# Kernel optimization log

Hardware: AMD Instinct MI355X
Metric: run time of the kernel (lower is better)

Reference implementation:

```python
import jax, jax.numpy as jnp
import numpy as np

NUM_HEADS = 16
ROPE_BASE = 10000.0


def _rope_cos_sin(T, head_dim, dtype):
    # standard rotary: angles[t, i] = t * base^(-2i/head_dim), half-split layout
    inv_freq = 1.0 / (ROPE_BASE ** (jnp.arange(0, head_dim, 2, dtype=jnp.float32) / head_dim))
    ang = jnp.arange(T, dtype=jnp.float32)[:, None] * inv_freq[None, :]  # [T, hd/2]
    cos = jnp.concatenate([jnp.cos(ang), jnp.cos(ang)], axis=-1).astype(dtype)  # [T, hd]
    sin = jnp.concatenate([jnp.sin(ang), jnp.sin(ang)], axis=-1).astype(dtype)
    return cos, sin


def _rotate_half(t):
    t1, t2 = jnp.split(t, 2, axis=-1)
    return jnp.concatenate([-t2, t1], axis=-1)


def _apply_rope(t, cos, sin):
    # t: [B, H, T, hd]; cos/sin: [T, hd]
    return t * cos[None, None] + _rotate_half(t) * sin[None, None]


def setup_inputs() -> dict:
    key = jax.random.key(0)
    B, T, C = 2, 2048, 1024
    k1, k2, k3 = jax.random.split(key, 3)
    x = jax.random.normal(k1, (B, T, C), dtype=jnp.float32)
    w_attn = jax.random.normal(k2, (C, 3 * C), dtype=jnp.float32) * (C ** -0.5)
    w_proj = jax.random.normal(k3, (C, C), dtype=jnp.float32) * (C ** -0.5)
    return {"x": x, "w_attn": w_attn, "w_proj": w_proj}


def reference(x, w_attn, w_proj):
    B, T, C = x.shape
    H = NUM_HEADS
    hd = C // H

    qkv = x @ w_attn  # [B, T, 3C]
    q, k, v = jnp.split(qkv, 3, axis=-1)
    # [B, T, C] -> [B, H, T, hd]
    q = q.reshape(B, T, H, hd).transpose(0, 2, 1, 3)
    k = k.reshape(B, T, H, hd).transpose(0, 2, 1, 3)
    v = v.reshape(B, T, H, hd).transpose(0, 2, 1, 3)

    cos, sin = _rope_cos_sin(T, hd, x.dtype)
    q = _apply_rope(q, cos, sin)
    k = _apply_rope(k, cos, sin)

    scale = 1.0 / np.sqrt(hd).astype(np.float32)
    att = jnp.einsum('bhqd,bhkd->bhqk', q, k) * scale  # [B, H, T, T]
    causal = jnp.tril(jnp.ones((T, T), dtype=bool))
    att = jnp.where(causal[None, None], att, jnp.array(-jnp.inf, dtype=att.dtype))
    att = jax.nn.softmax(att, axis=-1)
    y = jnp.einsum('bhqk,bhkd->bhqd', att, v)  # [B, H, T, hd]
    y = y.transpose(0, 2, 1, 3).reshape(B, T, C)
    return y @ w_proj
```

## Files before the change

### kernel.cpp

```cpp
#include <hip/hip_runtime.h>

typedef unsigned short u16;
typedef unsigned int u32;
typedef unsigned long long u64;
typedef __attribute__((ext_vector_type(8))) short s16x8;
typedef __attribute__((ext_vector_type(8))) __bf16 bf16x8;
typedef __attribute__((ext_vector_type(4))) float fx4;
typedef __attribute__((ext_vector_type(16))) float fx16;
typedef __attribute__((ext_vector_type(2))) u32 u32x2;
typedef __attribute__((ext_vector_type(4))) u32 u32x4;

__device__ __forceinline__ fx4 mfma_16x16x32(s16x8 a, s16x8 b, fx4 c) {
  return __builtin_amdgcn_mfma_f32_16x16x32_bf16(
      __builtin_bit_cast(bf16x8, a), __builtin_bit_cast(bf16x8, b), c, 0, 0, 0);
}
__device__ __forceinline__ fx16 mfma_32x32x16(s16x8 a, s16x8 b, fx16 c) {
  return __builtin_amdgcn_mfma_f32_32x32x16_bf16(
      __builtin_bit_cast(bf16x8, a), __builtin_bit_cast(bf16x8, b), c, 0, 0, 0);
}

__device__ __forceinline__ u16 f2bf(float f) {
  u32 u = __builtin_bit_cast(u32, f);
  u32 r = u + 0x7fffu + ((u >> 16) & 1u);
  return (u16)(r >> 16);
}
__device__ __forceinline__ float bf2f(u16 h) {
  u32 u = ((u32)h) << 16;
  return __builtin_bit_cast(float, u);
}

__device__ __forceinline__ u32 cvtpk(float lo, float hi) {
  u32 r;
  asm("v_cvt_pk_bf16_f32 %0, %1, %2" : "=v"(r) : "v"(lo), "v"(hi));
  return r;
}

__device__ __forceinline__ float max3f(float a, float b, float c) {
  float r;
  asm("v_max3_f32 %0, %1, %2, %3" : "=v"(r) : "v"(a), "v"(b), "v"(c));
  return r;
}

__device__ __forceinline__ void plswap(u32& x, u32& y) {
  typedef __attribute__((ext_vector_type(2))) unsigned int uix2;
  uix2 r = __builtin_amdgcn_permlane32_swap(x, y, false, false);
  x = r[0];
  y = r[1];
}

__device__ __forceinline__ float xhalf_max(float v) {
  u32 a = __builtin_bit_cast(u32, v), b = a;
  plswap(a, b);
  return fmaxf(__builtin_bit_cast(float, a), __builtin_bit_cast(float, b));
}
__device__ __forceinline__ float xhalf_sum(float v) {
  u32 a = __builtin_bit_cast(u32, v), b = a;
  plswap(a, b);
  return __builtin_bit_cast(float, a) + __builtin_bit_cast(float, b);
}

__device__ __forceinline__ void gload16(const void* g, void* l) {
  __builtin_amdgcn_global_load_lds(
      (const __attribute__((address_space(1))) u32*)g,
      (__attribute__((address_space(3))) u32*)l, 16, 0, 0);
}

#define B_ 2
#define T_ 2048
#define C_ 1024
#define H_ 16
#define HD_ 64
#define BH_ 32
#define M_ 4096
#define CF_ 0.18033688011112042f

__global__ __launch_bounds__(256) void prep_k(
    const float* __restrict__ x, const float* __restrict__ wa,
    const float* __restrict__ wp, u16* __restrict__ xb, u16* __restrict__ waT,
    u16* __restrict__ wpT, float* __restrict__ ct, float* __restrict__ st) {
  __shared__ u16 T_s[64 * 72];
  int b = blockIdx.x, tid = threadIdx.x;
  if (b < 2048) {
    int id = b * 256 + tid;
    const fx4* p = (const fx4*)(x + (u64)id * 8);
    fx4 v0 = p[0], v1 = p[1];
    s16x8 r;
#pragma unroll
    for (int j = 0; j < 4; ++j) {
      r[j] = (short)f2bf(v0[j]);
      r[4 + j] = (short)f2bf(v1[j]);
    }
    *((s16x8*)xb + id) = r;
  } else if (b < 3072) {
    const float* W;
    u16* WT;
    int Ncols, bx, by;
    if (b < 2816) {
      int i = b - 2048;
      W = wa; WT = waT; Ncols = 3072; bx = i % 48; by = i / 48;
    } else {
      int i = b - 2816;
      W = wp; WT = wpT; Ncols = 1024; bx = i % 16; by = i / 16;
    }
    int c0 = bx * 64, r0 = by * 64;
#pragma unroll
    for (int it = 0; it < 4; ++it) {
      int idx = it * 256 + tid;
      int r = idx >> 4, c4 = (idx & 15) * 4;
      fx4 v = *(const fx4*)(W + (u64)(r0 + r) * Ncols + c0 + c4);
#pragma unroll
      for (int j = 0; j < 4; ++j) T_s[(c4 + j) * 72 + r] = f2bf(v[j]);
    }
    __syncthreads();
#pragma unroll
    for (int it = 0; it < 2; ++it) {
      int idx = it * 256 + tid;
      int rc = idx >> 3, c8 = (idx & 7) * 8;
      s16x8 v = *(const s16x8*)(T_s + rc * 72 + c8);
      *(s16x8*)(WT + (u64)(c0 + rc) * 1024 + r0 + c8) = v;
    }
  } else {
    int id = (b - 3072) * 256 + tid;
    int t = id >> 5, i = id & 31;
    float f = exp2f(-(float)i * (13.287712379549449f / 32.0f));
    float a = (float)t * f;
    float s, c;
    sincosf(a, &s, &c);
    ct[id] = c;
    st[id] = s;
  }
}

__global__ __launch_bounds__(512, 2) void gemm1_8ph(
    const u16* __restrict__ A, const u16* __restrict__ B,
    u16* __restrict__ Qo, u16* __restrict__ Ko, u16* __restrict__ Vo,
    const float* __restrict__ ct, const float* __restrict__ st) {
  __shared__ u16 As[2][2][128 * 64];
  __shared__ u16 Bs[2][2][128 * 64];
  const int K = 1024;
  int tid = threadIdx.x, lane = tid & 63, w = tid >> 6;
  int wm = w >> 2, wn = w & 3, l15 = lane & 15, l4 = lane >> 4;
  int id = blockIdx.y * 12 + blockIdx.x;
  id = (id & 7) * 24 + (id >> 3);
  int m0 = (id / 12) * 256, n0 = (id % 12) * 256;

  const u16* asrc[2][2];
  const u16* bsrc[2][2];
  int dst16[2];
#pragma unroll
  for (int c = 0; c < 2; ++c) {
    int p = c * 512 + tid;
    int row = p >> 3, s = (p & 7) ^ (row & 7);
    dst16[c] = p * 16;
#pragma unroll
    for (int hh = 0; hh < 2; ++hh) {
      asrc[hh][c] = A + (u64)(m0 + hh * 128 + row) * K + s * 8;
      bsrc[hh][c] = B + (u64)(n0 + hh * 128 + row) * K + s * 8;
    }
  }

#define STAGE_A1(BUF, KOFF)                                               \
  do {                                                                    \
    _Pragma("unroll")                                                     \
    for (int hh_ = 0; hh_ < 2; ++hh_)                                     \
      _Pragma("unroll")                                                   \
      for (int c_ = 0; c_ < 2; ++c_)                                      \
        gload16(asrc[hh_][c_] + (KOFF), (char*)As[BUF][hh_] + dst16[c_]); \
  } while (0)
#define STAGE_B1(BUF, KOFF)                                               \
  do {                                                                    \
    _Pragma("unroll")                                                     \
    for (int hh_ = 0; hh_ < 2; ++hh_)                                     \
      _Pragma("unroll")                                                   \
      for (int c_ = 0; c_ < 2; ++c_)                                      \
        gload16(bsrc[hh_][c_] + (KOFF), (char*)Bs[BUF][hh_] + dst16[c_]); \
  } while (0)

#define RD_A(BUF, MI, KS)                                                  \
  (*(const s16x8*)((const char*)As[BUF][wm] +                              \
                   ((((MI)*16 + l15) * 8 +                                 \
                     (((KS)*4 + l4) ^ (l15 & 7))) * 16)))
#define RD_B(BUF, NJ, KS)                                                  \
  (*(const s16x8*)((const char*)Bs[BUF][wn >> 1] +                         \
                   ((((wn & 1) * 64 + (NJ)*16 + l15) * 8 +                 \
                     (((KS)*4 + l4) ^ (l15 & 7))) * 16)))

  fx4 acc[8][4] = {};

  STAGE_A1(0, 0);
  STAGE_B1(0, 0);
  asm volatile("s_waitcnt vmcnt(0)" ::: "memory");
  __builtin_amdgcn_s_barrier();
  __builtin_amdgcn_sched_barrier(0);

  for (int kt = 0; kt < 16; ++kt) {
    int buf = kt & 1;
    int ko = (kt + 1) * 64;
    s16x8 a[4], bb[4];
#pragma unroll
    for (int i = 0; i < 4; ++i) a[i] = RD_A(buf, i, 0);
#pragma unroll
    for (int j = 0; j < 4; ++j) bb[j] = RD_B(buf, j, 0);
    if (kt + 1 < 16) STAGE_A1(buf ^ 1, ko);
    __builtin_amdgcn_s_setprio(1);
#pragma unroll
    for (int i = 0; i < 4; ++i)
#pragma unroll
      for (int j = 0; j < 4; ++j)
        acc[i][j] = mfma_16x16x32(a[i], bb[j], acc[i][j]);
    __builtin_amdgcn_s_setprio(0);
    __builtin_amdgcn_s_barrier();
#pragma unroll
    for (int i = 0; i < 4; ++i) a[i] = RD_A(buf, 4 + i, 0);
    if (kt + 1 < 16) STAGE_B1(buf ^ 1, ko);
    __builtin_amdgcn_s_setprio(1);
#pragma unroll
    for (int i = 0; i < 4; ++i)
#pragma unroll
      for (int j = 0; j < 4; ++j)
        acc[4 + i][j] = mfma_16x16x32(a[i], bb[j], acc[4 + i][j]);
    __builtin_amdgcn_s_setprio(0);
    __builtin_amdgcn_s_barrier();
#pragma unroll
    for (int i = 0; i < 4; ++i) a[i] = RD_A(buf, i, 1);
#pragma unroll
    for (int j = 0; j < 4; ++j) bb[j] = RD_B(buf, j, 1);
    __builtin_amdgcn_s_setprio(1);
#pragma unroll
    for (int i = 0; i < 4; ++i)
#pragma unroll
      for (int j = 0; j < 4; ++j)
        acc[i][j] = mfma_16x16x32(a[i], bb[j], acc[i][j]);
    __builtin_amdgcn_s_setprio(0);
    __builtin_amdgcn_s_barrier();
#pragma unroll
    for (int i = 0; i < 4; ++i) a[i] = RD_A(buf, 4 + i, 1);
    __builtin_amdgcn_s_setprio(1);
#pragma unroll
    for (int i = 0; i < 4; ++i)
#pragma unroll
      for (int j = 0; j < 4; ++j)
        acc[4 + i][j] = mfma_16x16x32(a[i], bb[j], acc[4 + i][j]);
    __builtin_amdgcn_s_setprio(0);
    asm volatile("s_waitcnt vmcnt(0)" ::: "memory");
    __builtin_amdgcn_s_barrier();
    __builtin_amdgcn_sched_barrier(0);
  }
#undef STAGE_A1
#undef STAGE_B1
#undef RD_A
#undef RD_B

#pragma unroll
  for (int mi = 0; mi < 8; ++mi)
#pragma unroll
    for (int r = 0; r < 4; ++r) {
      int row = m0 + wm * 128 + mi * 16 + l4 * 4 + r;
      int b2 = row >> 11, t = row & (T_ - 1);
#pragma unroll
      for (int nj = 0; nj < 2; ++nj) {
        int col = n0 + wn * 64 + nj * 16 + l15;
        int qi = col >> 10, h = (col >> 6) & 15, d = nj * 16 + l15;
        float lo = acc[mi][nj][r], hi = acc[mi][nj + 2][r];
        if (qi == 2) {
          u64 vbase =
              ((((u64)(b2 * H_ + h)) * (T_ / 8) + (t >> 3)) * HD_ + d) * 8 + (t & 7);
          Vo[vbase] = f2bf(lo);
          Vo[vbase + 32 * 8] = f2bf(hi);
        } else {
          float c = ct[t * 32 + d], s = st[t * 32 + d];
          float sc = (qi == 0) ? CF_ : 1.0f;
          u16* dst = (qi == 0) ? Qo : Ko;
          u64 base = ((((u64)(b2 * H_ + h)) * 8 + (d >> 3)) * T_ + t) * 8 + (d & 7);
          dst[base] = f2bf((lo * c - hi * s) * sc);
          dst[base + (u64)4 * T_ * 8] = f2bf((hi * c + lo * s) * sc);
        }
      }
    }
}

__global__ __launch_bounds__(256, 3) void gemm2_k(
    const u16* __restrict__ A, const u16* __restrict__ B, float* __restrict__ C,
    int M, int N, int K) {
  __shared__ u16 AsS[3][128 * 32];
  __shared__ u16 BsS[3][128 * 32];
  int tid = threadIdx.x, lane = tid & 63, w = tid >> 6;
  int wm = w >> 1, wn = w & 1, l15 = lane & 15, l4 = lane >> 4;
  int nwg = gridDim.x * gridDim.y;
  int id = blockIdx.y * gridDim.x + blockIdx.x;
  int qq = nwg >> 3;
  id = (id & 7) * qq + (id >> 3);
  int m0 = (id / gridDim.x) * 128, n0 = (id % gridDim.x) * 128;
  fx4 acc[4][4] = {};

  const u16* asrc[2];
  const u16* bsrc[2];
#pragma unroll
  for (int g = 0; g < 2; ++g) {
    int idx = g * 256 + tid;
    int row = idx >> 2, slot = (idx & 3) ^ (row & 3);
    asrc[g] = A + (u64)(m0 + row) * K + slot * 8;
    bsrc[g] = B + (u64)(n0 + row) * K + slot * 8;
  }

#define GSTAGE(S, KOFF)                                                      \
  do {                                                                       \
    _Pragma("unroll")                                                        \
    for (int g_ = 0; g_ < 2; ++g_) {                                         \
      gload16(asrc[g_] + (KOFF), (char*)AsS[S] + g_ * 4096 + tid * 16);      \
      gload16(bsrc[g_] + (KOFF), (char*)BsS[S] + g_ * 4096 + tid * 16);      \
    }                                                                        \
  } while (0)

#define GCOMP(S)                                                             \
  do {                                                                       \
    s16x8 a_[4], b_[4];                                                      \
    _Pragma("unroll")                                                        \
    for (int mi_ = 0; mi_ < 4; ++mi_) {                                      \
      int r_ = wm * 64 + mi_ * 16 + l15;                                     \
      a_[mi_] = *(const s16x8*)((const char*)AsS[S] + r_ * 64 +              \
                                ((l4 ^ (r_ & 3)) * 16));                     \
    }                                                                        \
    _Pragma("unroll")                                                        \
    for (int ni_ = 0; ni_ < 4; ++ni_) {                                      \
      int r_ = wn * 64 + ni_ * 16 + l15;                                     \
      b_[ni_] = *(const s16x8*)((const char*)BsS[S] + r_ * 64 +              \
                                ((l4 ^ (r_ & 3)) * 16));                     \
    }                                                                        \
    _Pragma("unroll")                                                        \
    for (int mi_ = 0; mi_ < 4; ++mi_)                                        \
      _Pragma("unroll")                                                      \
      for (int ni_ = 0; ni_ < 4; ++ni_)                                      \
        acc[mi_][ni_] = mfma_16x16x32(a_[mi_], b_[ni_], acc[mi_][ni_]);      \
  } while (0)

  int NT = K >> 5;
  GSTAGE(0, 0);
  GSTAGE(1, 32);
  int s0 = 0, s1 = 1, s2 = 2;
  for (int t = 0; t < NT; ++t) {
    __builtin_amdgcn_s_barrier();
    __builtin_amdgcn_sched_barrier(0);
    if (t + 2 < NT) GSTAGE(s2, (t + 2) * 32);
    __builtin_amdgcn_sched_barrier(0);
    if (t < NT - 2)
      asm volatile("s_waitcnt vmcnt(8)" ::: "memory");
    else if (t == NT - 2)
      asm volatile("s_waitcnt vmcnt(4)" ::: "memory");
    else
      asm volatile("s_waitcnt vmcnt(0)" ::: "memory");
    __builtin_amdgcn_s_barrier();
    __builtin_amdgcn_sched_barrier(0);
    GCOMP(s0);
    int tmp = s0;
    s0 = s1;
    s1 = s2;
    s2 = tmp;
  }
#undef GSTAGE
#undef GCOMP

#pragma unroll
  for (int mi = 0; mi < 4; ++mi)
#pragma unroll
    for (int ni = 0; ni < 4; ++ni)
#pragma unroll
      for (int r = 0; r < 4; ++r) {
        u64 row = (u64)(m0 + wm * 64 + mi * 16 + l4 * 4 + r);
        int col = n0 + wn * 64 + ni * 16 + l15;
        C[row * N + col] = acc[mi][ni][r];
      }
}

#define LOADK(KC, KVI)                                                 \
  do {                                                                 \
    _Pragma("unroll")                                                  \
    for (int ks_ = 0; ks_ < 4; ++ks_)                                  \
      KC[ks_] = *(const s16x8*)(kp[ks_] + (u64)(KVI) * 256);           \
  } while (0)

#define LOADV(VC, KVI)                                                 \
  do {                                                                 \
    const u16* vk_ = vpb + (u64)(KVI) * 2048;                          \
    VC[0] = *(const s16x8*)(vk_);                                      \
    VC[1] = *(const s16x8*)(vk_ + 256);                                \
    VC[2] = *(const s16x8*)(vk_ + 1024);                               \
    VC[3] = *(const s16x8*)(vk_ + 1280);                               \
  } while (0)

#define ATTN_STEP(KC, VC, KVI)                                                \
  do {                                                                        \
    fx16 s_ = {};                                                             \
    __builtin_amdgcn_s_setprio(1);                                            \
    _Pragma("unroll")                                                         \
    for (int ks_ = 0; ks_ < 4; ++ks_)                                         \
      s_ = mfma_32x32x16(KC[ks_], qf[ks_], s_);                               \
    __builtin_amdgcn_s_setprio(0);                                            \
    if ((KVI) == jt) {                                                        \
      _Pragma("unroll")                                                       \
      for (int r_ = 0; r_ < 16; ++r_) {                                       \
        int cr_ = (r_ & 3) + 8 * (r_ >> 2) + 4 * h;                           \
        s_[r_] = (cr_ > ql) ? -1e30f : s_[r_];                                \
      }                                                                       \
    }                                                                         \
    float u0_ = max3f(s_[0], s_[1], s_[2]);                                   \
    float u1_ = max3f(s_[3], s_[4], s_[5]);                                   \
    float u2_ = max3f(s_[6], s_[7], s_[8]);                                   \
    float u3_ = max3f(s_[9], s_[10], s_[11]);                                 \
    float u4_ = max3f(s_[12], s_[13], s_[14]);                                \
    float v0_ = max3f(u0_, u1_, s_[15]);                                      \
    float v1_ = max3f(u2_, u3_, u4_);                                         \
    float rowmax_ = xhalf_max(fmaxf(v0_, v1_));                               \
    if (!__all(rowmax_ <= m + 8.f)) {                                         \
      float mnew_ = fmaxf(m, rowmax_);                                        \
      float corr_ = exp2f(m - mnew_);                                         \
      l *= corr_;                                                             \
      oL *= corr_;                                                            \
      oH *= corr_;                                                            \
      m = mnew_;                                                              \
    }                                                                         \
    float p_[16];                                                             \
    _Pragma("unroll")                                                         \
    for (int r_ = 0; r_ < 16; ++r_) p_[r_] = exp2f(s_[r_] - m);               \
    float a0_ = (p_[0] + p_[8]) + (p_[1] + p_[9]);                            \
    float a1_ = (p_[2] + p_[10]) + (p_[3] + p_[11]);                          \
    float a2_ = (p_[4] + p_[12]) + (p_[5] + p_[13]);                          \
    float a3_ = (p_[6] + p_[14]) + (p_[7] + p_[15]);                          \
    l += xhalf_sum((a0_ + a1_) + (a2_ + a3_));                                \
    u32 x0_ = cvtpk(p_[0], p_[1]), x1_ = cvtpk(p_[2], p_[3]);                 \
    u32 y0_ = cvtpk(p_[4], p_[5]), y1_ = cvtpk(p_[6], p_[7]);                 \
    plswap(x0_, y0_);                                                         \
    plswap(x1_, y1_);                                                         \
    u32x4 f0w_ = {x0_, x1_, y0_, y1_};                                        \
    u32 x2_ = cvtpk(p_[8], p_[9]), x3_ = cvtpk(p_[10], p_[11]);               \
    u32 y2_ = cvtpk(p_[12], p_[13]), y3_ = cvtpk(p_[14], p_[15]);             \
    plswap(x2_, y2_);                                                         \
    plswap(x3_, y3_);                                                         \
    u32x4 f1w_ = {x2_, x3_, y2_, y3_};                                        \
    s16x8 pf0_ = __builtin_bit_cast(s16x8, f0w_);                             \
    s16x8 pf1_ = __builtin_bit_cast(s16x8, f1w_);                             \
    __builtin_amdgcn_s_setprio(1);                                            \
    oL = mfma_32x32x16(VC[0], pf0_, oL);                                      \
    oH = mfma_32x32x16(VC[1], pf0_, oH);                                      \
    oL = mfma_32x32x16(VC[2], pf1_, oL);                                      \
    oH = mfma_32x32x16(VC[3], pf1_, oH);                                      \
    __builtin_amdgcn_s_setprio(0);                                            \
  } while (0)

#define OSTRIDE 68

__global__ __launch_bounds__(256, 3) void attn_fwd_k(
    const u16* __restrict__ Qp, const u16* __restrict__ Kp,
    const u16* __restrict__ Vp, u16* __restrict__ Y) {
  __shared__ float Ob[4 * 32 * OSTRIDE];
  __shared__ float Ml[4 * 32 * 2];
  int tid = threadIdx.x, lane = tid & 63, w = tid >> 6;
  int ql = lane & 31, h = lane >> 5;
  int bh = blockIdx.x & 31;
  int jt = 63 - (blockIdx.x >> 5);
  int q0 = jt * 32;
  int b2 = bh >> 4, head = bh & 15;
  int n = jt + 1;
  int lo = (w * n) >> 2, hi = ((w + 1) * n) >> 2;

  s16x8 qf[4];
#pragma unroll
  for (int ks = 0; ks < 4; ++ks)
    qf[ks] = *(const s16x8*)(Qp + (((u64)bh * 8 + ks * 2 + h) * T_ + q0 + ql) * 8);

  const u16* kp[4];
#pragma unroll
  for (int ks = 0; ks < 4; ++ks)
    kp[ks] = Kp + (((u64)bh * 8 + ks * 2 + h) * T_ + ql) * 8;
  const u16* vpb = Vp + (((u64)bh * (T_ / 8) + h) * HD_ + ql) * 8;

  fx16 oL = {}, oH = {};
  float m = -1e30f, l = 0.f;

  if (lo < hi) {
    s16x8 kA[4], vA[4], kB[4], vB[4];
    LOADK(kA, lo);
    LOADV(vA, lo);
    int kv = lo;
    for (; kv + 1 < hi; kv += 2) {
      LOADK(kB, kv + 1);
      LOADV(vB, kv + 1);
      ATTN_STEP(kA, vA, kv);
      if (kv + 2 < hi) {
        LOADK(kA, kv + 2);
        LOADV(vA, kv + 2);
      }
      ATTN_STEP(kB, vB, kv + 1);
    }
    if (kv < hi) ATTN_STEP(kA, vA, kv);
  }

  {
    float* ob = Ob + (w * 32 + ql) * OSTRIDE;
#pragma unroll
    for (int g = 0; g < 4; ++g) {
      fx4 a = {oL[4 * g], oL[4 * g + 1], oL[4 * g + 2], oL[4 * g + 3]};
      *(fx4*)(ob + 8 * g + 4 * h) = a;
      fx4 b = {oH[4 * g], oH[4 * g + 1], oH[4 * g + 2], oH[4 * g + 3]};
      *(fx4*)(ob + 32 + 8 * g + 4 * h) = b;
    }
    if (h == 0) {
      Ml[(w * 32 + ql) * 2] = m;
      Ml[(w * 32 + ql) * 2 + 1] = l;
    }
  }
  __syncthreads();

  {
    int q = tid >> 3, db = tid & 7;
    float mm0 = Ml[(0 * 32 + q) * 2], ll0 = Ml[(0 * 32 + q) * 2 + 1];
    float mm1 = Ml[(1 * 32 + q) * 2], ll1 = Ml[(1 * 32 + q) * 2 + 1];
    float mm2 = Ml[(2 * 32 + q) * 2], ll2 = Ml[(2 * 32 + q) * 2 + 1];
    float mm3 = Ml[(3 * 32 + q) * 2], ll3 = Ml[(3 * 32 + q) * 2 + 1];
    float mo = fmaxf(fmaxf(mm0, mm1), fmaxf(mm2, mm3));
    float w0 = exp2f(mm0 - mo), w1 = exp2f(mm1 - mo);
    float w2 = exp2f(mm2 - mo), w3 = exp2f(mm3 - mo);
    float rl = 1.0f / (ll0 * w0 + ll1 * w1 + ll2 * w2 + ll3 * w3);
    w0 *= rl; w1 *= rl; w2 *= rl; w3 *= rl;
    const float* ob = Ob + q * OSTRIDE + db * 8;
    fx4 aa = {}, bb = {};
#pragma unroll
    for (int i = 0; i < 4; ++i) {
      float wi = (i == 0) ? w0 : (i == 1) ? w1 : (i == 2) ? w2 : w3;
      fx4 pa = *(const fx4*)(ob + i * 32 * OSTRIDE);
      fx4 pb = *(const fx4*)(ob + i * 32 * OSTRIDE + 4);
      aa += wi * pa;
      bb += wi * pb;
    }
    u32x4 ow;
    ow[0] = cvtpk(aa[0], aa[1]);
    ow[1] = cvtpk(aa[2], aa[3]);
    ow[2] = cvtpk(bb[0], bb[1]);
    ow[3] = cvtpk(bb[2], bb[3]);
    int t = q0 + q;
    *(u32x4*)(Y + ((u64)(b2 * T_ + t)) * C_ + head * HD_ + db * 8) = ow;
  }
}

extern "C" void kernel_launch(void* const* d_in, const int* in_sizes, int n_in,
                              void* d_out, int out_size, void* d_ws, size_t ws_size,
                              hipStream_t stream) {
  (void)in_sizes; (void)n_in; (void)out_size; (void)ws_size;
  const float* x = (const float*)d_in[0];
  const float* w_attn = (const float*)d_in[1];
  const float* w_proj = (const float*)d_in[2];
  float* out = (float*)d_out;

  u16* xb = (u16*)d_ws;
  u16* waT = xb + (u64)M_ * C_;
  u16* wpT = waT + (u64)3 * C_ * C_;
  u16* Qp = wpT + (u64)C_ * C_;
  u16* Kp = Qp + (u64)BH_ * T_ * HD_;
  u16* Vp = Kp + (u64)BH_ * T_ * HD_;
  float* ct = (float*)(Vp + (u64)BH_ * T_ * HD_);
  float* st = ct + T_ * 32;
  u16* yb = xb;

  prep_k<<<3328, 256, 0, stream>>>(x, w_attn, w_proj, xb, waT, wpT, ct, st);

  gemm1_8ph<<<dim3(12, 16), 512, 0, stream>>>(xb, waT, Qp, Kp, Vp, ct, st);

  attn_fwd_k<<<2048, 256, 0, stream>>>(Qp, Kp, Vp, yb);

  gemm2_k<<<dim3(8, 32), 256, 0, stream>>>(yb, wpT, out, M_, C_, C_);
}
```

Measured before the change: 114.7 us.

## Replace QKV GEMM double buffer with a 10-slot LDS ring for deeper prefetch

The QKV projection GEMM drops its two-stage A/B shared-memory double buffer in favour of a 10-slot ring of 128x64 quarter tiles. A tiles are prefetched two K-steps ahead and B tiles one step ahead. The end-of-iteration wait relaxes from vmcnt(0) to vmcnt(4), so some global loads stay in flight across the barrier. The aim is to hide more global-load latency behind MFMA work, at the cost of more LDS (160KB versus 128KB), extra slot-index arithmetic, and a few redundant wrapped loads in the last iterations.

```diff
diff --git a/kernel.cpp b/kernel.cpp
--- a/kernel.cpp
+++ b/kernel.cpp
@@ -135,8 +135,7 @@
     const u16* __restrict__ A, const u16* __restrict__ B,
     u16* __restrict__ Qo, u16* __restrict__ Ko, u16* __restrict__ Vo,
     const float* __restrict__ ct, const float* __restrict__ st) {
-  __shared__ u16 As[2][2][128 * 64];
-  __shared__ u16 Bs[2][2][128 * 64];
+  __shared__ u16 ring[10 * 8192];
   const int K = 1024;
   int tid = threadIdx.x, lane = tid & 63, w = tid >> 6;
   int wm = w >> 2, wn = w & 3, l15 = lane & 15, l4 = lane >> 4;
@@ -144,64 +143,64 @@
   id = (id & 7) * 24 + (id >> 3);
   int m0 = (id / 12) * 256, n0 = (id % 12) * 256;
 
-  const u16* asrc[2][2];
-  const u16* bsrc[2][2];
-  int dst16[2];
+  const u16* srcA0[2];
+  const u16* srcA1[2];
+  const u16* srcB0[2];
+  const u16* srcB1[2];
+  int dstoff[2];
 #pragma unroll
   for (int c = 0; c < 2; ++c) {
     int p = c * 512 + tid;
     int row = p >> 3, s = (p & 7) ^ (row & 7);
-    dst16[c] = p * 16;
-#pragma unroll
-    for (int hh = 0; hh < 2; ++hh) {
-      asrc[hh][c] = A + (u64)(m0 + hh * 128 + row) * K + s * 8;
-      bsrc[hh][c] = B + (u64)(n0 + hh * 128 + row) * K + s * 8;
-    }
-  }
-
-#define STAGE_A1(BUF, KOFF)                                               \
-  do {                                                                    \
-    _Pragma("unroll")                                                     \
-    for (int hh_ = 0; hh_ < 2; ++hh_)                                     \
-      _Pragma("unroll")                                                   \
-      for (int c_ = 0; c_ < 2; ++c_)                                      \
-        gload16(asrc[hh_][c_] + (KOFF), (char*)As[BUF][hh_] + dst16[c_]); \
+    dstoff[c] = p * 16;
+    srcA0[c] = A + (u64)(m0 + row) * K + s * 8;
+    srcA1[c] = A + (u64)(m0 + 128 + row) * K + s * 8;
+    srcB0[c] = B + (u64)(n0 + row) * K + s * 8;
+    srcB1[c] = B + (u64)(n0 + 128 + row) * K + s * 8;
+  }
+
+  int slot_s = 0;
+
+#define STAGE_Q(SRC, KT)                                                    \
+  do {                                                                      \
+    int koff_ = ((KT) & 15) * 64;                                           \
+    char* base_ = (char*)ring + slot_s * 16384;                             \
+    gload16(SRC[0] + koff_, base_ + dstoff[0]);                             \
+    gload16(SRC[1] + koff_, base_ + dstoff[1]);                             \
+    slot_s = (slot_s == 9) ? 0 : slot_s + 1;                                \
   } while (0)
-#define STAGE_B1(BUF, KOFF)                                               \
-  do {                                                                    \
-    _Pragma("unroll")                                                     \
-    for (int hh_ = 0; hh_ < 2; ++hh_)                                     \
-      _Pragma("unroll")                                                   \
-      for (int c_ = 0; c_ < 2; ++c_)                                      \
-        gload16(bsrc[hh_][c_] + (KOFF), (char*)Bs[BUF][hh_] + dst16[c_]); \
-  } while (0)
-
-#define RD_A(BUF, MI, KS)                                                  \
-  (*(const s16x8*)((const char*)As[BUF][wm] +                              \
-                   ((((MI)*16 + l15) * 8 +                                 \
-                     (((KS)*4 + l4) ^ (l15 & 7))) * 16)))
-#define RD_B(BUF, NJ, KS)                                                  \
-  (*(const s16x8*)((const char*)Bs[BUF][wn >> 1] +                         \
-                   ((((wn & 1) * 64 + (NJ)*16 + l15) * 8 +                 \
-                     (((KS)*4 + l4) ^ (l15 & 7))) * 16)))
+
+#define RD_Q(BASE, ROW, KS)                                                 \
+  (*(const s16x8*)((const char*)(BASE) +                                    \
+                   (((ROW)*8 + (((KS)*4 + l4) ^ (l15 & 7))) * 16)))
 
   fx4 acc[8][4] = {};
 
-  STAGE_A1(0, 0);
-  STAGE_B1(0, 0);
-  asm volatile("s_waitcnt vmcnt(0)" ::: "memory");
+  STAGE_Q(srcA0, 0);
+  STAGE_Q(srcA1, 0);
+  STAGE_Q(srcB0, 0);
+  STAGE_Q(srcB1, 0);
+  STAGE_Q(srcA0, 1);
+  STAGE_Q(srcA1, 1);
+  asm volatile("s_waitcnt vmcnt(4)" ::: "memory");
   __builtin_amdgcn_s_barrier();
   __builtin_amdgcn_sched_barrier(0);
 
-  for (int kt = 0; kt < 16; ++kt) {
-    int buf = kt & 1;
-    int ko = (kt + 1) * 64;
+  int bt = 0;
+  for (int t = 0; t < 16; ++t) {
+    int sA = bt + wm;
+    if (sA >= 10) sA -= 10;
+    int sB = bt + 2 + (wn >> 1);
+    if (sB >= 10) sB -= 10;
+    const char* Ab = (const char*)ring + sA * 16384;
+    const char* Bb = (const char*)ring + sB * 16384;
     s16x8 a[4], bb[4];
 #pragma unroll
-    for (int i = 0; i < 4; ++i) a[i] = RD_A(buf, i, 0);
-#pragma unroll
-    for (int j = 0; j < 4; ++j) bb[j] = RD_B(buf, j, 0);
-    if (kt + 1 < 16) STAGE_A1(buf ^ 1, ko);
+    for (int i = 0; i < 4; ++i) a[i] = RD_Q(Ab, i * 16 + l15, 0);
+#pragma unroll
+    for (int j = 0; j < 4; ++j)
+      bb[j] = RD_Q(Bb, (wn & 1) * 64 + j * 16 + l15, 0);
+    STAGE_Q(srcB0, t + 1);
     __builtin_amdgcn_s_setprio(1);
 #pragma unroll
     for (int i = 0; i < 4; ++i)
@@ -211,8 +210,8 @@
     __builtin_amdgcn_s_setprio(0);
     __builtin_amdgcn_s_barrier();
 #pragma unroll
-    for (int i = 0; i < 4; ++i) a[i] = RD_A(buf, 4 + i, 0);
-    if (kt + 1 < 16) STAGE_B1(buf ^ 1, ko);
+    for (int i = 0; i < 4; ++i) a[i] = RD_Q(Ab, (4 + i) * 16 + l15, 0);
+    STAGE_Q(srcB1, t + 1);
     __builtin_amdgcn_s_setprio(1);
 #pragma unroll
     for (int i = 0; i < 4; ++i)
@@ -222,9 +221,11 @@
     __builtin_amdgcn_s_setprio(0);
     __builtin_amdgcn_s_barrier();
 #pragma unroll
-    for (int i = 0; i < 4; ++i) a[i] = RD_A(buf, i, 1);
-#pragma unroll
-    for (int j = 0; j < 4; ++j) bb[j] = RD_B(buf, j, 1);
+    for (int i = 0; i < 4; ++i) a[i] = RD_Q(Ab, i * 16 + l15, 1);
+#pragma unroll
+    for (int j = 0; j < 4; ++j)
+      bb[j] = RD_Q(Bb, (wn & 1) * 64 + j * 16 + l15, 1);
+    STAGE_Q(srcA0, t + 2);
     __builtin_amdgcn_s_setprio(1);
 #pragma unroll
     for (int i = 0; i < 4; ++i)
@@ -234,7 +235,8 @@
     __builtin_amdgcn_s_setprio(0);
     __builtin_amdgcn_s_barrier();
 #pragma unroll
-    for (int i = 0; i < 4; ++i) a[i] = RD_A(buf, 4 + i, 1);
+    for (int i = 0; i < 4; ++i) a[i] = RD_Q(Ab, (4 + i) * 16 + l15, 1);
+    STAGE_Q(srcA1, t + 2);
     __builtin_amdgcn_s_setprio(1);
 #pragma unroll
     for (int i = 0; i < 4; ++i)
@@ -242,14 +244,14 @@
       for (int j = 0; j < 4; ++j)
         acc[4 + i][j] = mfma_16x16x32(a[i], bb[j], acc[4 + i][j]);
     __builtin_amdgcn_s_setprio(0);
-    asm volatile("s_waitcnt vmcnt(0)" ::: "memory");
+    asm volatile("s_waitcnt vmcnt(4)" ::: "memory");
     __builtin_amdgcn_s_barrier();
     __builtin_amdgcn_sched_barrier(0);
-  }
-#undef STAGE_A1
-#undef STAGE_B1
-#undef RD_A
-#undef RD_B
+    bt += 4;
+    if (bt >= 10) bt -= 10;
+  }
+#undef STAGE_Q
+#undef RD_Q
 
 #pragma unroll
   for (int mi = 0; mi < 8; ++mi)
```

Measured after the change: 112.5 us. No clear change (-1.9%).
